# Performance work log

Measured on AMD Instinct MI355X. Metric: run time of the kernel, lower is better.

## Reference

```python
import jax, jax.numpy as jnp
import numpy as np

KSIZE = 3        # kernel_size
SW = 4           # spatial_groups = (1, 4): blocks along width only
KBITS = 4        # fake-quant bits for the kernel


def fake_quant_weights(w, num_bits=KBITS):
    # per-tensor symmetric fake quant with straight-through estimator
    qmax = float(2 ** (num_bits - 1) - 1)  # 7 for 4 bits
    scale = jnp.max(jnp.abs(w)) / qmax
    q = jnp.round(w / scale) * scale
    return w + jax.lax.stop_gradient(q - w)


def setup_inputs() -> dict:
    key = jax.random.key(0)
    k1, k2 = jax.random.split(key, 2)
    N, C, H, W, F = 32, 64, 56, 56, 128
    inputs = jax.random.normal(k1, (N, C, H, W), dtype=jnp.float32)
    # glorot_uniform over (fan_in = k*k*C, fan_out = F)
    fan_in = KSIZE * KSIZE * C
    limit = float(np.sqrt(6.0 / (fan_in + F)))
    kernel = jax.random.uniform(k2, (1, SW, fan_in, F), dtype=jnp.float32,
                                minval=-limit, maxval=limit)
    bias = jnp.zeros((F,), dtype=jnp.float32)
    return {"inputs": inputs, "kernel": kernel, "bias": bias}


def reference(inputs, kernel, bias):
    # inputs: [N, C, H, W]; kernel: [1, SW, C*K*K, F]; bias: [F]
    N, C, H, W = inputs.shape
    F = kernel.shape[-1]
    qk = fake_quant_weights(kernel, KBITS)[0]          # [SW, C*K*K, F]

    xp = jnp.pad(inputs, ((0, 0), (0, 0), (1, 1), (1, 1)))  # pad H,W by 1
    # im2col: patch flattened over (C, kh, kw), matching K.local_conv NCHW
    # patches: [N, C, K*K, H, W] -> [N, C*K*K, H, W]
    patches = jnp.stack(
        [xp[:, :, i:i + H, j:j + W] for i in range(KSIZE) for j in range(KSIZE)],
        axis=2,
    ).reshape(N, C * KSIZE * KSIZE, H, W)

    # split output columns into SW contiguous blocks of width W//SW,
    # each block uses its own weight matrix (w_interval = (W+2)//SW = W//SW here)
    Wb = W // SW
    p = patches.reshape(N, C * KSIZE * KSIZE, H, SW, Wb)   # [N, P, H, SW, Wb]
    out = jnp.einsum('nphbw,bpf->nfhbw', p, qk)            # [N, F, H, SW, Wb]
    out = out.reshape(N, F, H, W) + bias[None, :, None, None]
    return out
```

## Files before the change

### kernel.cpp

```cpp
#include <hip/hip_runtime.h>
#include <hip/hip_bf16.h>

#define CIN   64
#define HH_   56
#define WW_   56
#define FOUT  128
#define NN    32
#define SW    4
#define WB    14
#define HB    14
#define NW    (SW*9*FOUT*CIN)
#define QWT_PER_B (8*9*2*64*8)

typedef __attribute__((ext_vector_type(8))) short bf16x8;
typedef __attribute__((ext_vector_type(4))) float f32x4;

__device__ inline unsigned short f2bf(float x) {
    unsigned u = __float_as_uint(x);
    return (unsigned short)((u + 0x7FFFu + ((u >> 16) & 1u)) >> 16);
}

__global__ void absmax_part(const float* __restrict__ w, float* __restrict__ part) {
    __shared__ float sm[4];
    int tid = threadIdx.x;
    float m = 0.f;
    for (int idx = blockIdx.x * 256 + tid; idx < NW; idx += 64 * 256)
        m = fmaxf(m, fabsf(w[idx]));
    #pragma unroll
    for (int off = 32; off > 0; off >>= 1)
        m = fmaxf(m, __shfl_down(m, off, 64));
    if ((tid & 63) == 0) sm[tid >> 6] = m;
    __syncthreads();
    if (tid == 0)
        part[blockIdx.x] = fmaxf(fmaxf(sm[0], sm[1]), fmaxf(sm[2], sm[3]));
}

__global__ void quant_pack(const float* __restrict__ w, const float* __restrict__ part,
                           unsigned short* __restrict__ qwt) {
    float pm = part[threadIdx.x & 63];
    #pragma unroll
    for (int off = 1; off < 64; off <<= 1)
        pm = fmaxf(pm, __shfl_xor(pm, off, 64));
    float scale = pm / 7.0f;
    int o = blockIdx.x * 256 + threadIdx.x;
    if (o >= NW) return;
    int r    = o & 7;
    int lane = (o >> 3) & 63;
    int cc   = (o >> 9) & 1;
    int idx  = o >> 10;
    int t    = idx % 9;
    int ft   = (idx / 9) & 7;
    int b    = idx / 72;
    int f = ft * 16 + (lane & 15);
    int c = cc * 32 + (lane >> 4) * 8 + r;
    float v = w[((b * CIN + c) * 9 + t) * FOUT + f];
    qwt[o] = f2bf(rintf(v / scale) * scale);
}

__global__ __launch_bounds__(512, 2)
void conv_mfma(const float* __restrict__ in,
               const unsigned short* __restrict__ qwt,
               const float* __restrict__ bias,
               float* __restrict__ out) {
    const int hgb = blockIdx.x, n = blockIdx.y, b = blockIdx.z;
    const int h0 = hgb * HB, w0 = b * WB;
    const int tid = threadIdx.x;
    const int wave = tid >> 6, lane = tid & 63;
    const int q = lane >> 4, lm = lane & 15;
    const int wf = wave >> 1, wp = wave & 1;

    __shared__ __align__(16) unsigned short s_slab[256 * 64];

    const unsigned short* wbase = qwt + (size_t)b * QWT_PER_B + lane * 8;
    bf16x8 wt[2][9][2];
    #pragma unroll
    for (int m = 0; m < 2; ++m)
        #pragma unroll
        for (int t = 0; t < 9; ++t)
            #pragma unroll
            for (int cc = 0; cc < 2; ++cc)
                wt[m][t][cc] = *(const bf16x8*)&wbase[((((wf * 2 + m) * 9) + t) * 2 + cc) * 512];

    #pragma unroll
    for (int i = 0; i < 16; ++i) {
        int e = i * 512 + tid;
        int cp  = e & 15;
        int c0  = ((e >> 4) & 31) * 2;
        int row = e >> 9;
        int hi = h0 - 1 + row, wi = w0 - 1 + cp;
        float v0 = 0.f, v1 = 0.f;
        if (hi >= 0 && hi < HH_ && wi >= 0 && wi < WW_) {
            const float* p = &in[((n * CIN + c0) * HH_ + hi) * WW_ + wi];
            v0 = p[0]; v1 = p[HH_ * WW_];
        }
        unsigned pk = (unsigned)f2bf(v0) | ((unsigned)f2bf(v1) << 16);
        int pix = row * 16 + cp;
        *(unsigned*)&s_slab[pix * 64 + (c0 ^ ((cp & 7) << 3))] = pk;
    }
    __syncthreads();

    f32x4 acc[2][7];
    #pragma unroll
    for (int m = 0; m < 2; ++m)
        #pragma unroll
        for (int p = 0; p < 7; ++p)
            acc[m][p] = (f32x4){0.f, 0.f, 0.f, 0.f};

    #pragma unroll
    for (int t = 0; t < 9; ++t) {
        const int kh = t / 3, kw = t - (t / 3) * 3;
        const int sc  = (lm + kw) & 15;
        const int swz = (sc & 7) << 3;
        #pragma unroll
        for (int cc = 0; cc < 2; ++cc) {
            const int koff = cc * 32 + q * 8;
            bf16x8 bfr[7];
            #pragma unroll
            for (int p = 0; p < 7; ++p) {
                int srow = wp * 7 + p + kh;
                bfr[p] = *(const bf16x8*)&s_slab[(srow * 16 + sc) * 64 + (koff ^ swz)];
            }
            #pragma unroll
            for (int m = 0; m < 2; ++m)
                #pragma unroll
                for (int p = 0; p < 7; ++p)
                    acc[m][p] = __builtin_amdgcn_mfma_f32_16x16x32_bf16(
                        wt[m][t][cc], bfr[p], acc[m][p], 0, 0, 0);
        }
    }

    if (lm < WB) {
        #pragma unroll
        for (int m = 0; m < 2; ++m) {
            #pragma unroll
            for (int r = 0; r < 4; ++r) {
                int f = (wf * 2 + m) * 16 + q * 4 + r;
                float bv = bias[f];
                float* op = &out[(((size_t)n * FOUT + f) * HH_ + h0 + wp * 7) * WW_ + w0 + lm];
                #pragma unroll
                for (int p = 0; p < 7; ++p)
                    op[p * WW_] = acc[m][p][r] + bv;
            }
        }
    }
}

extern "C" void kernel_launch(void* const* d_in, const int* in_sizes, int n_in,
                              void* d_out, int out_size, void* d_ws, size_t ws_size,
                              hipStream_t stream) {
    const float* inputs = (const float*)d_in[0];
    const float* kernel = (const float*)d_in[1];
    const float* bias   = (const float*)d_in[2];
    float* out          = (float*)d_out;

    float*          part = (float*)d_ws;
    unsigned short* qwt  = (unsigned short*)((char*)d_ws + 512);

    absmax_part<<<64, 256, 0, stream>>>(kernel, part);
    quant_pack<<<(NW + 255) / 256, 256, 0, stream>>>(kernel, part, qwt);

    dim3 grid(HH_ / HB, NN, SW);
    conv_mfma<<<grid, 512, 0, stream>>>(inputs, qwt, bias, out);
}
```

Baseline: 117.9 us.

## Process two row tiles per block and prefetch second input slab during compute

Each block now handles two consecutive 14-row tiles instead of one, halving the grid. Weight registers are loaded once per block and reused across both tiles. The second tile's input is loaded into registers before the first tile's MFMA loop, then written to a second LDS buffer afterwards, so global load latency overlaps compute. The costs are doubled LDS (64 KB per block), which may reduce occupancy, 64 extra live registers, and a grid of only 256 blocks that may underfill the GPU.

```diff
diff --git a/kernel.cpp b/kernel.cpp
--- a/kernel.cpp
+++ b/kernel.cpp
@@ -62,14 +62,15 @@
                const unsigned short* __restrict__ qwt,
                const float* __restrict__ bias,
                float* __restrict__ out) {
-    const int hgb = blockIdx.x, n = blockIdx.y, b = blockIdx.z;
-    const int h0 = hgb * HB, w0 = b * WB;
+    const int hp = blockIdx.x, n = blockIdx.y, b = blockIdx.z;
+    const int w0 = b * WB;
+    const int h0a = hp * 2 * HB, h0b = h0a + HB;
     const int tid = threadIdx.x;
     const int wave = tid >> 6, lane = tid & 63;
     const int q = lane >> 4, lm = lane & 15;
     const int wf = wave >> 1, wp = wave & 1;
 
-    __shared__ __align__(16) unsigned short s_slab[256 * 64];
+    __shared__ __align__(16) unsigned short s_slab[2][256 * 64];
 
     const unsigned short* wbase = qwt + (size_t)b * QWT_PER_B + lane * 8;
     bf16x8 wt[2][9][2];
@@ -81,23 +82,78 @@
             for (int cc = 0; cc < 2; ++cc)
                 wt[m][t][cc] = *(const bf16x8*)&wbase[((((wf * 2 + m) * 9) + t) * 2 + cc) * 512];
 
-    #pragma unroll
-    for (int i = 0; i < 16; ++i) {
-        int e = i * 512 + tid;
-        int cp  = e & 15;
-        int c0  = ((e >> 4) & 31) * 2;
-        int row = e >> 9;
-        int hi = h0 - 1 + row, wi = w0 - 1 + cp;
-        float v0 = 0.f, v1 = 0.f;
-        if (hi >= 0 && hi < HH_ && wi >= 0 && wi < WW_) {
-            const float* p = &in[((n * CIN + c0) * HH_ + hi) * WW_ + wi];
-            v0 = p[0]; v1 = p[HH_ * WW_];
+    auto stage_load = [&](int h0, float (&r0)[16], float (&r1)[16]) {
+        #pragma unroll
+        for (int i = 0; i < 16; ++i) {
+            int e = i * 512 + tid;
+            int cp = e & 15, c0 = ((e >> 4) & 31) * 2, row = e >> 9;
+            int hi = h0 - 1 + row, wi = w0 - 1 + cp;
+            float v0 = 0.f, v1 = 0.f;
+            if (hi >= 0 && hi < HH_ && wi >= 0 && wi < WW_) {
+                const float* p = &in[((n * CIN + c0) * HH_ + hi) * WW_ + wi];
+                v0 = p[0]; v1 = p[HH_ * WW_];
+            }
+            r0[i] = v0; r1[i] = v1;
         }
-        unsigned pk = (unsigned)f2bf(v0) | ((unsigned)f2bf(v1) << 16);
-        int pix = row * 16 + cp;
-        *(unsigned*)&s_slab[pix * 64 + (c0 ^ ((cp & 7) << 3))] = pk;
-    }
-    __syncthreads();
+    };
+    auto stage_write = [&](int bi, float (&r0)[16], float (&r1)[16]) {
+        #pragma unroll
+        for (int i = 0; i < 16; ++i) {
+            int e = i * 512 + tid;
+            int cp = e & 15, c0 = ((e >> 4) & 31) * 2, row = e >> 9;
+            unsigned pk = (unsigned)f2bf(r0[i]) | ((unsigned)f2bf(r1[i]) << 16);
+            int pix = row * 16 + cp;
+            *(unsigned*)&s_slab[bi][pix * 64 + (c0 ^ ((cp & 7) << 3))] = pk;
+        }
+    };
+    auto kloop = [&](int bi, f32x4 (&acc)[2][7]) {
+        #pragma unroll
+        for (int t = 0; t < 9; ++t) {
+            const int kh = t / 3, kw = t - (t / 3) * 3;
+            const int sc  = (lm + kw) & 15;
+            const int swz = (sc & 7) << 3;
+            #pragma unroll
+            for (int cc = 0; cc < 2; ++cc) {
+                const int koff = cc * 32 + q * 8;
+                bf16x8 bfr[7];
+                #pragma unroll
+                for (int p = 0; p < 7; ++p) {
+                    int srow = wp * 7 + p + kh;
+                    bfr[p] = *(const bf16x8*)&s_slab[bi][(srow * 16 + sc) * 64 + (koff ^ swz)];
+                }
+                #pragma unroll
+                for (int m = 0; m < 2; ++m)
+                    #pragma unroll
+                    for (int p = 0; p < 7; ++p)
+                        acc[m][p] = __builtin_amdgcn_mfma_f32_16x16x32_bf16(
+                            wt[m][t][cc], bfr[p], acc[m][p], 0, 0, 0);
+            }
+        }
+    };
+    auto epilogue = [&](int h0, f32x4 (&acc)[2][7]) {
+        if (lm < WB) {
+            #pragma unroll
+            for (int m = 0; m < 2; ++m) {
+                #pragma unroll
+                for (int r = 0; r < 4; ++r) {
+                    int f = (wf * 2 + m) * 16 + q * 4 + r;
+                    float bv = bias[f];
+                    float* op = &out[(((size_t)n * FOUT + f) * HH_ + h0 + wp * 7) * WW_ + w0 + lm];
+                    #pragma unroll
+                    for (int p = 0; p < 7; ++p)
+                        op[p * WW_] = acc[m][p][r] + bv;
+                }
+            }
+        }
+    };
+
+    float va0[16], va1[16], vb0[16], vb1[16];
+    stage_load(h0a, va0, va1);
+    stage_write(0, va0, va1);
+    stage_load(h0b, vb0, vb1);
+
+    asm volatile("s_waitcnt lgkmcnt(0)" ::: "memory");
+    __builtin_amdgcn_s_barrier();
 
     f32x4 acc[2][7];
     #pragma unroll
@@ -106,43 +162,21 @@
         for (int p = 0; p < 7; ++p)
             acc[m][p] = (f32x4){0.f, 0.f, 0.f, 0.f};
 
+    kloop(0, acc);
+    epilogue(h0a, acc);
+
     #pragma unroll
-    for (int t = 0; t < 9; ++t) {
-        const int kh = t / 3, kw = t - (t / 3) * 3;
-        const int sc  = (lm + kw) & 15;
-        const int swz = (sc & 7) << 3;
+    for (int m = 0; m < 2; ++m)
         #pragma unroll
-        for (int cc = 0; cc < 2; ++cc) {
-            const int koff = cc * 32 + q * 8;
-            bf16x8 bfr[7];
-            #pragma unroll
-            for (int p = 0; p < 7; ++p) {
-                int srow = wp * 7 + p + kh;
-                bfr[p] = *(const bf16x8*)&s_slab[(srow * 16 + sc) * 64 + (koff ^ swz)];
-            }
-            #pragma unroll
-            for (int m = 0; m < 2; ++m)
-                #pragma unroll
-                for (int p = 0; p < 7; ++p)
-                    acc[m][p] = __builtin_amdgcn_mfma_f32_16x16x32_bf16(
-                        wt[m][t][cc], bfr[p], acc[m][p], 0, 0, 0);
-        }
-    }
+        for (int p = 0; p < 7; ++p)
+            acc[m][p] = (f32x4){0.f, 0.f, 0.f, 0.f};
 
-    if (lm < WB) {
-        #pragma unroll
-        for (int m = 0; m < 2; ++m) {
-            #pragma unroll
-            for (int r = 0; r < 4; ++r) {
-                int f = (wf * 2 + m) * 16 + q * 4 + r;
-                float bv = bias[f];
-                float* op = &out[(((size_t)n * FOUT + f) * HH_ + h0 + wp * 7) * WW_ + w0 + lm];
-                #pragma unroll
-                for (int p = 0; p < 7; ++p)
-                    op[p * WW_] = acc[m][p][r] + bv;
-            }
-        }
-    }
+    stage_write(1, vb0, vb1);
+    asm volatile("s_waitcnt lgkmcnt(0)" ::: "memory");
+    __builtin_amdgcn_s_barrier();
+
+    kloop(1, acc);
+    epilogue(h0b, acc);
 }
 
 extern "C" void kernel_launch(void* const* d_in, const int* in_sizes, int n_in,
@@ -159,6 +193,6 @@
     absmax_part<<<64, 256, 0, stream>>>(kernel, part);
     quant_pack<<<(NW + 255) / 256, 256, 0, stream>>>(kernel, part, qwt);
 
-    dim3 grid(HH_ / HB, NN, SW);
+    dim3 grid(2, NN, SW);
     conv_mfma<<<grid, 512, 0, stream>>>(inputs, qwt, bias, out);
 }
```

New measurement: 146.4 us. +24.2%, slower.

## Process two row-blocks per workgroup to amortize weight register loads

Applied to the files above, without the earlier changes.

Each conv workgroup now handles two 14-row blocks instead of one, staging both input slabs in shared memory (doubling LDS to 64KB) and halving the grid to 256 workgroups. The per-lane weight fragments are loaded once and reused across both blocks, and an empty asm barrier pins them in VGPRs so the compiler does not rematerialize the loads. This trades fewer redundant weight loads and more work per block for lower occupancy and fewer workgroups across the CUs.

```diff
diff --git a/kernel.cpp b/kernel.cpp
--- a/kernel.cpp
+++ b/kernel.cpp
@@ -62,14 +62,15 @@
                const unsigned short* __restrict__ qwt,
                const float* __restrict__ bias,
                float* __restrict__ out) {
-    const int hgb = blockIdx.x, n = blockIdx.y, b = blockIdx.z;
-    const int h0 = hgb * HB, w0 = b * WB;
+    const int hp = blockIdx.x, n = blockIdx.y, b = blockIdx.z;
+    const int w0 = b * WB;
+    const int h0a = hp * 2 * HB, h0b = h0a + HB;
     const int tid = threadIdx.x;
     const int wave = tid >> 6, lane = tid & 63;
     const int q = lane >> 4, lm = lane & 15;
     const int wf = wave >> 1, wp = wave & 1;
 
-    __shared__ __align__(16) unsigned short s_slab[256 * 64];
+    __shared__ __align__(16) unsigned short s_slab[2][256 * 64];
 
     const unsigned short* wbase = qwt + (size_t)b * QWT_PER_B + lane * 8;
     bf16x8 wt[2][9][2];
@@ -82,64 +83,82 @@
                 wt[m][t][cc] = *(const bf16x8*)&wbase[((((wf * 2 + m) * 9) + t) * 2 + cc) * 512];
 
     #pragma unroll
-    for (int i = 0; i < 16; ++i) {
-        int e = i * 512 + tid;
-        int cp  = e & 15;
-        int c0  = ((e >> 4) & 31) * 2;
-        int row = e >> 9;
-        int hi = h0 - 1 + row, wi = w0 - 1 + cp;
-        float v0 = 0.f, v1 = 0.f;
-        if (hi >= 0 && hi < HH_ && wi >= 0 && wi < WW_) {
-            const float* p = &in[((n * CIN + c0) * HH_ + hi) * WW_ + wi];
-            v0 = p[0]; v1 = p[HH_ * WW_];
+    for (int s = 0; s < 2; ++s) {
+        const int h0 = s ? h0b : h0a;
+        #pragma unroll
+        for (int i = 0; i < 16; ++i) {
+            int e = i * 512 + tid;
+            int cp = e & 15, c0 = ((e >> 4) & 31) * 2, row = e >> 9;
+            int hi = h0 - 1 + row, wi = w0 - 1 + cp;
+            float v0 = 0.f, v1 = 0.f;
+            if (hi >= 0 && hi < HH_ && wi >= 0 && wi < WW_) {
+                const float* p = &in[((n * CIN + c0) * HH_ + hi) * WW_ + wi];
+                v0 = p[0]; v1 = p[HH_ * WW_];
+            }
+            unsigned pk = (unsigned)f2bf(v0) | ((unsigned)f2bf(v1) << 16);
+            int pix = row * 16 + cp;
+            *(unsigned*)&s_slab[s][pix * 64 + (c0 ^ ((cp & 7) << 3))] = pk;
         }
-        unsigned pk = (unsigned)f2bf(v0) | ((unsigned)f2bf(v1) << 16);
-        int pix = row * 16 + cp;
-        *(unsigned*)&s_slab[pix * 64 + (c0 ^ ((cp & 7) << 3))] = pk;
     }
+
+    #pragma unroll
+    for (int m = 0; m < 2; ++m)
+        #pragma unroll
+        for (int t = 0; t < 9; ++t)
+            #pragma unroll
+            for (int cc = 0; cc < 2; ++cc) {
+                f32x4 tmp = __builtin_bit_cast(f32x4, wt[m][t][cc]);
+                asm volatile("" : "+v"(tmp));
+                wt[m][t][cc] = __builtin_bit_cast(bf16x8, tmp);
+            }
+
     __syncthreads();
 
     f32x4 acc[2][7];
     #pragma unroll
-    for (int m = 0; m < 2; ++m)
+    for (int s = 0; s < 2; ++s) {
         #pragma unroll
-        for (int p = 0; p < 7; ++p)
-            acc[m][p] = (f32x4){0.f, 0.f, 0.f, 0.f};
+        for (int m = 0; m < 2; ++m)
+            #pragma unroll
+            for (int p = 0; p < 7; ++p)
+                acc[m][p] = (f32x4){0.f, 0.f, 0.f, 0.f};
 
-    #pragma unroll
-    for (int t = 0; t < 9; ++t) {
-        const int kh = t / 3, kw = t - (t / 3) * 3;
-        const int sc  = (lm + kw) & 15;
-        const int swz = (sc & 7) << 3;
         #pragma unroll
-        for (int cc = 0; cc < 2; ++cc) {
-            const int koff = cc * 32 + q * 8;
-            bf16x8 bfr[7];
+        for (int t = 0; t < 9; ++t) {
+            const int kh = t / 3, kw = t - (t / 3) * 3;
+            const int sc  = (lm + kw) & 15;
+            const int swz = (sc & 7) << 3;
             #pragma unroll
-            for (int p = 0; p < 7; ++p) {
-                int srow = wp * 7 + p + kh;
-                bfr[p] = *(const bf16x8*)&s_slab[(srow * 16 + sc) * 64 + (koff ^ swz)];
+            for (int cc = 0; cc < 2; ++cc) {
+                const int koff = cc * 32 + q * 8;
+                bf16x8 bfr[7];
+                #pragma unroll
+                for (int p = 0; p < 7; ++p) {
+                    int srow = wp * 7 + p + kh;
+                    bfr[p] = *(const bf16x8*)&s_slab[s][(srow * 16 + sc) * 64 + (koff ^ swz)];
+                }
+                #pragma unroll
+                for (int m = 0; m < 2; ++m)
+                    #pragma unroll
+                    for (int p = 0; p < 7; ++p)
+                        acc[m][p] = __builtin_amdgcn_mfma_f32_16x16x32_bf16(
+                            wt[m][t][cc], bfr[p], acc[m][p], 0, 0, 0);
             }
+        }
+
+        const int h0 = s ? h0b : h0a;
+        if (lm < WB) {
             #pragma unroll
-            for (int m = 0; m < 2; ++m)
+            for (int m = 0; m < 2; ++m) {
                 #pragma unroll
-                for (int p = 0; p < 7; ++p)
-                    acc[m][p] = __builtin_amdgcn_mfma_f32_16x16x32_bf16(
-                        wt[m][t][cc], bfr[p], acc[m][p], 0, 0, 0);
-        }
-    }
-
-    if (lm < WB) {
-        #pragma unroll
-        for (int m = 0; m < 2; ++m) {
-            #pragma unroll
-            for (int r = 0; r < 4; ++r) {
-                int f = (wf * 2 + m) * 16 + q * 4 + r;
-                float bv = bias[f];
-                float* op = &out[(((size_t)n * FOUT + f) * HH_ + h0 + wp * 7) * WW_ + w0 + lm];
-                #pragma unroll
-                for (int p = 0; p < 7; ++p)
-                    op[p * WW_] = acc[m][p][r] + bv;
+                for (int r = 0; r < 4; ++r) {
+                    int f = (wf * 2 + m) * 16 + q * 4 + r;
+                    float bv = bias[f];
+                    float* op = &out[(((size_t)n * FOUT + f) * HH_ + h0 + wp * 7) * WW_ + w0 + lm];
+                    #pragma unroll
+                    for (int p = 0; p < 7; ++p)
+                        op[p * WW_] = acc[m][p][r] + bv;
+                }
             }
         }
     }
@@ -159,6 +178,6 @@
     absmax_part<<<64, 256, 0, stream>>>(kernel, part);
     quant_pack<<<(NW + 255) / 256, 256, 0, stream>>>(kernel, part, qwt);
 
-    dim3 grid(HH_ / HB, NN, SW);
+    dim3 grid(2, NN, SW);
     conv_mfma<<<grid, 512, 0, stream>>>(inputs, qwt, bias, out);
 }
```

Measured after the change: 120.9 us. +2.6%, slower.
